# Optimization experiments

Measured on AMD Instinct MI355X. Metric: run time of the kernel, lower is better.

Reference implementation:

```python
import jax, jax.numpy as jnp
import numpy as np

HIDDEN = 1024
NUM_HEADS = 16
HEAD_DIM = HIDDEN // NUM_HEADS


def setup_inputs() -> dict:
    key = jax.random.key(0)
    ks = jax.random.split(key, 9)
    s = 0.02
    return {
        "x": jax.random.normal(ks[0], (2, 2048, HIDDEN), dtype=jnp.float32),
        "wq": jax.random.normal(ks[1], (HIDDEN, HIDDEN), dtype=jnp.float32) * s,
        "bq": jnp.zeros((HIDDEN,), dtype=jnp.float32),
        "wk": jax.random.normal(ks[2], (HIDDEN, HIDDEN), dtype=jnp.float32) * s,
        "bk": jnp.zeros((HIDDEN,), dtype=jnp.float32),
        "wv": jax.random.normal(ks[3], (HIDDEN, HIDDEN), dtype=jnp.float32) * s,
        "bv": jnp.zeros((HIDDEN,), dtype=jnp.float32),
        "wo": jax.random.normal(ks[4], (HIDDEN, HIDDEN), dtype=jnp.float32) * s,
        "bo": jnp.zeros((HIDDEN,), dtype=jnp.float32),
    }


def reference(x, wq, bq, wk, bk, wv, bv, wo, bo):
    B, S, H = x.shape
    # torch nn.Linear: y = x @ W.T + b
    q = x @ wq.T + bq
    k = x @ wk.T + bk
    v = x @ wv.T + bv
    # [B, S, nH, dH] -> [B, nH, S, dH]
    q = q.reshape(B, S, NUM_HEADS, HEAD_DIM).transpose(0, 2, 1, 3)
    k = k.reshape(B, S, NUM_HEADS, HEAD_DIM).transpose(0, 2, 1, 3)
    v = v.reshape(B, S, NUM_HEADS, HEAD_DIM).transpose(0, 2, 1, 3)
    scores = jnp.einsum("bhqd,bhkd->bhqk", q, k)
    probs = jax.nn.softmax(scores / jnp.sqrt(jnp.float32(HEAD_DIM)), axis=-1)
    context = jnp.einsum("bhqk,bhkd->bhqd", probs, v)
    context = context.transpose(0, 2, 1, 3).reshape(B, S, H)
    return context @ wo.T + bo
```

## Files before the change

### kernel.cpp

```cpp
#include <hip/hip_runtime.h>
#include <math.h>

#define HID   1024
#define NHEAD 16
#define DHEAD 64
#define BATCH 2
#define SEQ   2048
#define TOK   (BATCH*SEQ)

typedef float f32x4  __attribute__((ext_vector_type(4)));
typedef short short8 __attribute__((ext_vector_type(8)));

__device__ __forceinline__ unsigned short f2bf(float f) {
    unsigned int u = __float_as_uint(f);
    u += 0x7FFFu + ((u >> 16) & 1u);
    return (unsigned short)(u >> 16);
}

__global__ __launch_bounds__(256) void cvt_bf16(const float* __restrict__ in,
                                                unsigned short* __restrict__ out, int n8) {
    int i = blockIdx.x * 256 + threadIdx.x;
    if (i >= n8) return;
    const float4* p = (const float4*)in;
    float4 a = p[2*i], b = p[2*i+1];
    uint4 r;
    r.x = (unsigned)f2bf(a.x) | ((unsigned)f2bf(a.y) << 16);
    r.y = (unsigned)f2bf(a.z) | ((unsigned)f2bf(a.w) << 16);
    r.z = (unsigned)f2bf(b.x) | ((unsigned)f2bf(b.y) << 16);
    r.w = (unsigned)f2bf(b.z) | ((unsigned)f2bf(b.w) << 16);
    ((uint4*)out)[i] = r;
}

template<int NZ, bool OUTF32>
__global__ __launch_bounds__(256) void gemm128(
    const unsigned short* __restrict__ A,
    const unsigned short* __restrict__ W0, const unsigned short* __restrict__ W1,
    const unsigned short* __restrict__ W2,
    const float* __restrict__ b0, const float* __restrict__ b1, const float* __restrict__ b2,
    void* __restrict__ C0, void* __restrict__ C1, void* __restrict__ C2,
    int M, int N, int K)
{
    __shared__ unsigned short As[128][40];
    __shared__ unsigned short Ws[128][40];
    const unsigned short* W = W0; const float* bias = b0; void* C = C0;
    if (NZ > 1) {
        int z = blockIdx.z;
        W    = (z==0) ? W0 : ((z==1) ? W1 : W2);
        bias = (z==0) ? b0 : ((z==1) ? b1 : b2);
        C    = (z==0) ? C0 : ((z==1) ? C1 : C2);
    }
    const int tid  = threadIdx.x;
    const int l15  = tid & 15, quad = (tid >> 4) & 3, w = tid >> 6;
    const int wm   = (w >> 1) * 64, wn = (w & 1) * 64;
    const int m0   = blockIdx.y * 128, n0 = blockIdx.x * 128;
    const int sr   = tid >> 2, sc = (tid & 3) * 8;

    f32x4 acc[4][4] = {};

    for (int k0 = 0; k0 < K; k0 += 32) {
        uint4 a0 = *(const uint4*)(A + (size_t)(m0+sr   )*K + k0 + sc);
        uint4 a1 = *(const uint4*)(A + (size_t)(m0+sr+64)*K + k0 + sc);
        uint4 w0 = *(const uint4*)(W + (size_t)(n0+sr   )*K + k0 + sc);
        uint4 w1 = *(const uint4*)(W + (size_t)(n0+sr+64)*K + k0 + sc);
        __syncthreads();
        *(uint4*)&As[sr   ][sc] = a0;
        *(uint4*)&As[sr+64][sc] = a1;
        *(uint4*)&Ws[sr   ][sc] = w0;
        *(uint4*)&Ws[sr+64][sc] = w1;
        __syncthreads();
        short8 af[4], bfv[4];
        #pragma unroll
        for (int mi = 0; mi < 4; ++mi) af[mi]  = *(const short8*)&As[wm + mi*16 + l15][quad*8];
        #pragma unroll
        for (int ni = 0; ni < 4; ++ni) bfv[ni] = *(const short8*)&Ws[wn + ni*16 + l15][quad*8];
        #pragma unroll
        for (int mi = 0; mi < 4; ++mi)
            #pragma unroll
            for (int ni = 0; ni < 4; ++ni)
                acc[mi][ni] = __builtin_amdgcn_mfma_f32_16x16x32_bf16(af[mi], bfv[ni], acc[mi][ni], 0, 0, 0);
    }

    float bv[4];
    #pragma unroll
    for (int ni = 0; ni < 4; ++ni) bv[ni] = bias[n0 + wn + ni*16 + l15];
    #pragma unroll
    for (int mi = 0; mi < 4; ++mi)
        #pragma unroll
        for (int ni = 0; ni < 4; ++ni)
            #pragma unroll
            for (int r = 0; r < 4; ++r) {
                const int row = m0 + wm + mi*16 + quad*4 + r;
                const int col = n0 + wn + ni*16 + l15;
                const float val = acc[mi][ni][r] + bv[ni];
                if (OUTF32) ((float*)C)[(size_t)row*N + col] = val;
                else ((unsigned short*)C)[(size_t)row*N + col] = f2bf(val);
            }
}

__global__ __launch_bounds__(256) void attn_mfma(
    const unsigned short* __restrict__ Qg, const unsigned short* __restrict__ Kg,
    const unsigned short* __restrict__ Vg, unsigned short* __restrict__ Og)
{
    __shared__ unsigned short Qs[128][72];
    __shared__ unsigned short Ks[64][72];
    __shared__ unsigned short VT[64][72];
    __shared__ unsigned short Pw[4][32][72];

    const int tid  = threadIdx.x;
    const int l15  = tid & 15, quad = (tid >> 4) & 3, w = tid >> 6;
    const int b    = blockIdx.z, h = blockIdx.y;
    const int q0   = blockIdx.x * 128;
    const size_t rowbase = (size_t)b * SEQ;
    const int    cbase   = h * DHEAD;

    {
        const int r = tid >> 1, c = (tid & 1) * 32;
        const unsigned short* src = Qg + (rowbase + q0 + r) * HID + cbase + c;
        *(uint4*)&Qs[r][c     ] = *(const uint4*)(src);
        *(uint4*)&Qs[r][c +  8] = *(const uint4*)(src + 8);
        *(uint4*)&Qs[r][c + 16] = *(const uint4*)(src + 16);
        *(uint4*)&Qs[r][c + 24] = *(const uint4*)(src + 24);
    }
    __syncthreads();

    short8 qa[2][2];
    #pragma unroll
    for (int mi = 0; mi < 2; ++mi)
        #pragma unroll
        for (int slab = 0; slab < 2; ++slab)
            qa[mi][slab] = *(const short8*)&Qs[w*32 + mi*16 + l15][slab*32 + quad*8];

    f32x4 o[2][4] = {};
    float l_acc[2][4] = {};

    for (int kt = 0; kt < SEQ/64; ++kt) {
        __syncthreads();
        {
            const int r = tid >> 2, c = (tid & 3) * 16;
            const unsigned short* src = Kg + (rowbase + kt*64 + r) * HID + cbase + c;
            *(uint4*)&Ks[r][c    ] = *(const uint4*)src;
            *(uint4*)&Ks[r][c + 8] = *(const uint4*)(src + 8);
        }
        {
            const int d = tid & 63;
            #pragma unroll
            for (int p = 0; p < 2; ++p) {
                const int kk = ((tid >> 6) * 8) + p * 32;
                const unsigned short* src = Vg + (rowbase + kt*64 + kk) * HID + cbase + d;
                unsigned int pk[4];
                #pragma unroll
                for (int j = 0; j < 4; ++j) {
                    unsigned int lo = src[(size_t)(2*j    ) * HID];
                    unsigned int hi = src[(size_t)(2*j + 1) * HID];
                    pk[j] = lo | (hi << 16);
                }
                uint4 v4; v4.x = pk[0]; v4.y = pk[1]; v4.z = pk[2]; v4.w = pk[3];
                *(uint4*)&VT[d][kk] = v4;
            }
        }
        __syncthreads();

        f32x4 s[2][4] = {};
        #pragma unroll
        for (int slab = 0; slab < 2; ++slab) {
            short8 kf[4];
            #pragma unroll
            for (int nt = 0; nt < 4; ++nt)
                kf[nt] = *(const short8*)&Ks[nt*16 + l15][slab*32 + quad*8];
            #pragma unroll
            for (int mi = 0; mi < 2; ++mi)
                #pragma unroll
                for (int nt = 0; nt < 4; ++nt)
                    s[mi][nt] = __builtin_amdgcn_mfma_f32_16x16x32_bf16(qa[mi][slab], kf[nt], s[mi][nt], 0, 0, 0);
        }

        #pragma unroll
        for (int mi = 0; mi < 2; ++mi)
            #pragma unroll
            for (int nt = 0; nt < 4; ++nt) {
                const f32x4 sv = s[mi][nt];
                #pragma unroll
                for (int r = 0; r < 4; ++r) {
                    const float p = __expf(sv[r] * 0.125f);
                    l_acc[mi][r] += p;
                    Pw[w][mi*16 + quad*4 + r][nt*16 + l15] = f2bf(p);
                }
            }

        #pragma unroll
        for (int slab = 0; slab < 2; ++slab) {
            short8 pa[2], vf[4];
            #pragma unroll
            for (int mi = 0; mi < 2; ++mi)
                pa[mi] = *(const short8*)&Pw[w][mi*16 + l15][slab*32 + quad*8];
            #pragma unroll
            for (int nt = 0; nt < 4; ++nt)
                vf[nt] = *(const short8*)&VT[nt*16 + l15][slab*32 + quad*8];
            #pragma unroll
            for (int mi = 0; mi < 2; ++mi)
                #pragma unroll
                for (int nt = 0; nt < 4; ++nt)
                    o[mi][nt] = __builtin_amdgcn_mfma_f32_16x16x32_bf16(pa[mi], vf[nt], o[mi][nt], 0, 0, 0);
        }
    }

    float linv[2][4];
    #pragma unroll
    for (int mi = 0; mi < 2; ++mi)
        #pragma unroll
        for (int r = 0; r < 4; ++r) {
            float l = l_acc[mi][r];
            l += __shfl_xor(l, 1, 16);
            l += __shfl_xor(l, 2, 16);
            l += __shfl_xor(l, 4, 16);
            l += __shfl_xor(l, 8, 16);
            linv[mi][r] = 1.0f / l;
        }
    #pragma unroll
    for (int mi = 0; mi < 2; ++mi)
        #pragma unroll
        for (int nt = 0; nt < 4; ++nt)
            #pragma unroll
            for (int r = 0; r < 4; ++r) {
                const size_t row = rowbase + q0 + w*32 + mi*16 + quad*4 + r;
                Og[row * HID + cbase + nt*16 + l15] = f2bf(o[mi][nt][r] * linv[mi][r]);
            }
}

extern "C" void kernel_launch(void* const* d_in, const int* in_sizes, int n_in,
                              void* d_out, int out_size, void* d_ws, size_t ws_size,
                              hipStream_t stream)
{
    const float* x  = (const float*)d_in[0];
    const float* wq = (const float*)d_in[1];
    const float* bq = (const float*)d_in[2];
    const float* wk = (const float*)d_in[3];
    const float* bk = (const float*)d_in[4];
    const float* wv = (const float*)d_in[5];
    const float* bv = (const float*)d_in[6];
    const float* wo = (const float*)d_in[7];
    const float* bo = (const float*)d_in[8];
    float* out = (float*)d_out;

    unsigned short* xb  = (unsigned short*)d_ws;
    unsigned short* wqb = xb  + (size_t)TOK * HID;
    unsigned short* wkb = wqb + (size_t)HID * HID;
    unsigned short* wvb = wkb + (size_t)HID * HID;
    unsigned short* wob = wvb + (size_t)HID * HID;
    unsigned short* qb  = wob + (size_t)HID * HID;
    unsigned short* kb  = qb  + (size_t)TOK * HID;
    unsigned short* vb  = kb  + (size_t)TOK * HID;
    unsigned short* cb  = vb  + (size_t)TOK * HID;

    const dim3 blk(256);
    cvt_bf16<<<dim3(TOK*HID/8/256), blk, 0, stream>>>(x,  xb,  TOK*HID/8);
    cvt_bf16<<<dim3(HID*HID/8/256), blk, 0, stream>>>(wq, wqb, HID*HID/8);
    cvt_bf16<<<dim3(HID*HID/8/256), blk, 0, stream>>>(wk, wkb, HID*HID/8);
    cvt_bf16<<<dim3(HID*HID/8/256), blk, 0, stream>>>(wv, wvb, HID*HID/8);
    cvt_bf16<<<dim3(HID*HID/8/256), blk, 0, stream>>>(wo, wob, HID*HID/8);

    gemm128<3, false><<<dim3(HID/128, TOK/128, 3), blk, 0, stream>>>(
        xb, wqb, wkb, wvb, bq, bk, bv, qb, kb, vb, TOK, HID, HID);

    attn_mfma<<<dim3(SEQ/128, NHEAD, BATCH), blk, 0, stream>>>(qb, kb, vb, cb);

    gemm128<1, true><<<dim3(HID/128, TOK/128, 1), blk, 0, stream>>>(
        cb, wob, wob, wob, bo, bo, bo, out, out, out, TOK, HID, HID);
}
```

Baseline: 237.7 us.

## Rework GEMM with direct LDS loads and attention with pre-transposed V, double buffering

The GEMM now stages tiles with global_load_lds into XOR-swizzled shared memory instead of going through registers. The QKV GEMM writes V pre-transposed per head so attention can load it with vector reads. Attention processes 256 queries per block with double-buffered K/V prefetch, swizzled LDS layouts and packed P writes via lane shuffles. The four weight conversions are merged into one launch. The attention grid shrinks to 256 blocks at one block per CU, which risks under-filling the device, and the new swizzled index math could hide correctness problems.

```diff
diff --git a/kernel.cpp b/kernel.cpp
--- a/kernel.cpp
+++ b/kernel.cpp
@@ -1,4 +1,5 @@
 #include <hip/hip_runtime.h>
+#include <hip/hip_bf16.h>
 #include <math.h>
 
 #define HID   1024
@@ -15,6 +16,18 @@
     unsigned int u = __float_as_uint(f);
     u += 0x7FFFu + ((u >> 16) & 1u);
     return (unsigned short)(u >> 16);
+}
+
+__device__ __forceinline__ unsigned pk2(float lo, float hi) {
+    union { __hip_bfloat162 h; unsigned u; } cv;
+    cv.h = __float22bfloat162_rn(make_float2(lo, hi));
+    return cv.u;
+}
+
+__device__ __forceinline__ void gll16(const unsigned short* g, unsigned short* l) {
+    __builtin_amdgcn_global_load_lds(
+        (const __attribute__((address_space(1))) void*)g,
+        (__attribute__((address_space(3))) void*)l, 16, 0, 0);
 }
 
 __global__ __launch_bounds__(256) void cvt_bf16(const float* __restrict__ in,
@@ -24,15 +37,31 @@
     const float4* p = (const float4*)in;
     float4 a = p[2*i], b = p[2*i+1];
     uint4 r;
-    r.x = (unsigned)f2bf(a.x) | ((unsigned)f2bf(a.y) << 16);
-    r.y = (unsigned)f2bf(a.z) | ((unsigned)f2bf(a.w) << 16);
-    r.z = (unsigned)f2bf(b.x) | ((unsigned)f2bf(b.y) << 16);
-    r.w = (unsigned)f2bf(b.z) | ((unsigned)f2bf(b.w) << 16);
+    r.x = pk2(a.x, a.y); r.y = pk2(a.z, a.w);
+    r.z = pk2(b.x, b.y); r.w = pk2(b.z, b.w);
     ((uint4*)out)[i] = r;
 }
 
+__global__ __launch_bounds__(256) void cvt_bf16_w4(
+    const float* __restrict__ i0, const float* __restrict__ i1,
+    const float* __restrict__ i2, const float* __restrict__ i3,
+    unsigned short* __restrict__ o0, unsigned short* __restrict__ o1,
+    unsigned short* __restrict__ o2, unsigned short* __restrict__ o3, int n8) {
+    int i = blockIdx.x * 256 + threadIdx.x;
+    if (i >= n8) return;
+    int z = blockIdx.y;
+    const float* in = (z==0)?i0:((z==1)?i1:((z==2)?i2:i3));
+    unsigned short* out = (z==0)?o0:((z==1)?o1:((z==2)?o2:o3));
+    const float4* p = (const float4*)in;
+    float4 a = p[2*i], b = p[2*i+1];
+    uint4 r;
+    r.x = pk2(a.x, a.y); r.y = pk2(a.z, a.w);
+    r.z = pk2(b.x, b.y); r.w = pk2(b.z, b.w);
+    ((uint4*)out)[i] = r;
+}
+
 template<int NZ, bool OUTF32>
-__global__ __launch_bounds__(256) void gemm128(
+__global__ __launch_bounds__(256, 3) void gemm_gll(
     const unsigned short* __restrict__ A,
     const unsigned short* __restrict__ W0, const unsigned short* __restrict__ W1,
     const unsigned short* __restrict__ W2,
@@ -40,11 +69,13 @@
     void* __restrict__ C0, void* __restrict__ C1, void* __restrict__ C2,
     int M, int N, int K)
 {
-    __shared__ unsigned short As[128][40];
-    __shared__ unsigned short Ws[128][40];
+    __shared__ unsigned short As[128*32];
+    __shared__ unsigned short Ws[128*32];
+
     const unsigned short* W = W0; const float* bias = b0; void* C = C0;
+    int z = 0;
     if (NZ > 1) {
-        int z = blockIdx.z;
+        z = blockIdx.z;
         W    = (z==0) ? W0 : ((z==1) ? W1 : W2);
         bias = (z==0) ? b0 : ((z==1) ? b1 : b2);
         C    = (z==0) ? C0 : ((z==1) ? C1 : C2);
@@ -53,163 +84,209 @@
     const int l15  = tid & 15, quad = (tid >> 4) & 3, w = tid >> 6;
     const int wm   = (w >> 1) * 64, wn = (w & 1) * 64;
     const int m0   = blockIdx.y * 128, n0 = blockIdx.x * 128;
-    const int sr   = tid >> 2, sc = (tid & 3) * 8;
+
+    const int lane = tid & 63, w4 = tid >> 6;
+    const int grow = lane >> 2;
+    const int gchk = (lane & 3) ^ (grow & 3);
+    const unsigned short* pa0 = A + (size_t)(m0      + w4*16 + grow) * K + gchk*8;
+    const unsigned short* pa1 = A + (size_t)(m0 + 64 + w4*16 + grow) * K + gchk*8;
+    const unsigned short* pw0 = W + (size_t)(n0      + w4*16 + grow) * K + gchk*8;
+    const unsigned short* pw1 = W + (size_t)(n0 + 64 + w4*16 + grow) * K + gchk*8;
+    unsigned short* lA0 = &As[(w4*16)      * 32];
+    unsigned short* lA1 = &As[(64 + w4*16) * 32];
+    unsigned short* lW0 = &Ws[(w4*16)      * 32];
+    unsigned short* lW1 = &Ws[(64 + w4*16) * 32];
+
+    const int rchk = ((l15 & 3) );
 
     f32x4 acc[4][4] = {};
 
     for (int k0 = 0; k0 < K; k0 += 32) {
-        uint4 a0 = *(const uint4*)(A + (size_t)(m0+sr   )*K + k0 + sc);
-        uint4 a1 = *(const uint4*)(A + (size_t)(m0+sr+64)*K + k0 + sc);
-        uint4 w0 = *(const uint4*)(W + (size_t)(n0+sr   )*K + k0 + sc);
-        uint4 w1 = *(const uint4*)(W + (size_t)(n0+sr+64)*K + k0 + sc);
+        gll16(pa0, lA0); gll16(pa1, lA1);
+        gll16(pw0, lW0); gll16(pw1, lW1);
+        pa0 += 32; pa1 += 32; pw0 += 32; pw1 += 32;
         __syncthreads();
-        *(uint4*)&As[sr   ][sc] = a0;
-        *(uint4*)&As[sr+64][sc] = a1;
-        *(uint4*)&Ws[sr   ][sc] = w0;
-        *(uint4*)&Ws[sr+64][sc] = w1;
-        __syncthreads();
+
         short8 af[4], bfv[4];
-        #pragma unroll
-        for (int mi = 0; mi < 4; ++mi) af[mi]  = *(const short8*)&As[wm + mi*16 + l15][quad*8];
-        #pragma unroll
-        for (int ni = 0; ni < 4; ++ni) bfv[ni] = *(const short8*)&Ws[wn + ni*16 + l15][quad*8];
+        const int co = (quad ^ rchk) * 8;
+        #pragma unroll
+        for (int mi = 0; mi < 4; ++mi) af[mi]  = *(const short8*)&As[(wm + mi*16 + l15)*32 + co];
+        #pragma unroll
+        for (int ni = 0; ni < 4; ++ni) bfv[ni] = *(const short8*)&Ws[(wn + ni*16 + l15)*32 + co];
         #pragma unroll
         for (int mi = 0; mi < 4; ++mi)
             #pragma unroll
             for (int ni = 0; ni < 4; ++ni)
                 acc[mi][ni] = __builtin_amdgcn_mfma_f32_16x16x32_bf16(af[mi], bfv[ni], acc[mi][ni], 0, 0, 0);
+        __syncthreads();
     }
 
     float bv[4];
     #pragma unroll
     for (int ni = 0; ni < 4; ++ni) bv[ni] = bias[n0 + wn + ni*16 + l15];
-    #pragma unroll
-    for (int mi = 0; mi < 4; ++mi)
-        #pragma unroll
-        for (int ni = 0; ni < 4; ++ni)
-            #pragma unroll
-            for (int r = 0; r < 4; ++r) {
-                const int row = m0 + wm + mi*16 + quad*4 + r;
-                const int col = n0 + wn + ni*16 + l15;
-                const float val = acc[mi][ni][r] + bv[ni];
-                if (OUTF32) ((float*)C)[(size_t)row*N + col] = val;
-                else ((unsigned short*)C)[(size_t)row*N + col] = f2bf(val);
+
+    if (NZ == 3 && z == 2) {
+        #pragma unroll
+        for (int mi = 0; mi < 4; ++mi)
+            #pragma unroll
+            for (int ni = 0; ni < 4; ++ni) {
+                const int row0 = m0 + wm + mi*16 + quad*4;
+                const int col  = n0 + wn + ni*16 + l15;
+                const int hh = col >> 6, dd = col & 63;
+                const int bb = row0 >> 11, ss = row0 & 2047;
+                ushort4 r4;
+                r4.x = f2bf(acc[mi][ni][0] + bv[ni]);
+                r4.y = f2bf(acc[mi][ni][1] + bv[ni]);
+                r4.z = f2bf(acc[mi][ni][2] + bv[ni]);
+                r4.w = f2bf(acc[mi][ni][3] + bv[ni]);
+                *(ushort4*)((unsigned short*)C + ((size_t)(bb*NHEAD + hh)*DHEAD + dd)*SEQ + ss) = r4;
             }
-}
-
-__global__ __launch_bounds__(256) void attn_mfma(
+    } else {
+        #pragma unroll
+        for (int mi = 0; mi < 4; ++mi)
+            #pragma unroll
+            for (int ni = 0; ni < 4; ++ni)
+                #pragma unroll
+                for (int r = 0; r < 4; ++r) {
+                    const int row = m0 + wm + mi*16 + quad*4 + r;
+                    const int col = n0 + wn + ni*16 + l15;
+                    const float val = acc[mi][ni][r] + bv[ni];
+                    if (OUTF32) ((float*)C)[(size_t)row*N + col] = val;
+                    else ((unsigned short*)C)[(size_t)row*N + col] = f2bf(val);
+                }
+    }
+}
+
+__global__ __launch_bounds__(256, 1) void attn_v3(
     const unsigned short* __restrict__ Qg, const unsigned short* __restrict__ Kg,
-    const unsigned short* __restrict__ Vg, unsigned short* __restrict__ Og)
+    const unsigned short* __restrict__ vT, unsigned short* __restrict__ Og)
 {
-    __shared__ unsigned short Qs[128][72];
-    __shared__ unsigned short Ks[64][72];
-    __shared__ unsigned short VT[64][72];
-    __shared__ unsigned short Pw[4][32][72];
+    __shared__ unsigned short Ks[2][64][64];
+    __shared__ unsigned short VT[2][64][64];
+    __shared__ unsigned short Pw[4][64][64];
+    unsigned short* Qs = &Pw[0][0][0];
 
     const int tid  = threadIdx.x;
     const int l15  = tid & 15, quad = (tid >> 4) & 3, w = tid >> 6;
     const int b    = blockIdx.z, h = blockIdx.y;
-    const int q0   = blockIdx.x * 128;
+    const int q0   = blockIdx.x * 256;
     const size_t rowbase = (size_t)b * SEQ;
     const int    cbase   = h * DHEAD;
+    const size_t vbase   = (size_t)(b*NHEAD + h) * DHEAD * SEQ;
 
     {
-        const int r = tid >> 1, c = (tid & 1) * 32;
-        const unsigned short* src = Qg + (rowbase + q0 + r) * HID + cbase + c;
-        *(uint4*)&Qs[r][c     ] = *(const uint4*)(src);
-        *(uint4*)&Qs[r][c +  8] = *(const uint4*)(src + 8);
-        *(uint4*)&Qs[r][c + 16] = *(const uint4*)(src + 16);
-        *(uint4*)&Qs[r][c + 24] = *(const uint4*)(src + 24);
-    }
-    __syncthreads();
-
-    short8 qa[2][2];
+        const unsigned short* src = Qg + (rowbase + q0 + tid) * HID + cbase;
+        #pragma unroll
+        for (int j = 0; j < 8; ++j)
+            *(uint4*)&Qs[tid*64 + ((j ^ (tid & 7)) * 8)] = *(const uint4*)(src + j*8);
+    }
+    short8 qa[4][2];
     #pragma unroll
-    for (int mi = 0; mi < 2; ++mi)
-        #pragma unroll
-        for (int slab = 0; slab < 2; ++slab)
-            qa[mi][slab] = *(const short8*)&Qs[w*32 + mi*16 + l15][slab*32 + quad*8];
-
-    f32x4 o[2][4] = {};
-    float l_acc[2][4] = {};
+    for (int mi = 0; mi < 4; ++mi)
+        #pragma unroll
+        for (int s2 = 0; s2 < 2; ++s2)
+            qa[mi][s2] = *(const short8*)&Qs[(w*64 + mi*16 + l15)*64 + (((s2*4 + quad) ^ (l15 & 7)) * 8)];
+
+    const int sr = tid >> 2, sc = (tid & 3) * 16;
+    const int c0 = (sc >> 3) ^ (sr & 7);
+    const int c1 = ((sc >> 3) + 1) ^ (sr & 7);
+    {
+        const unsigned short* ks = Kg + (rowbase + sr) * HID + cbase + sc;
+        const unsigned short* vs = vT + vbase + (size_t)sr * SEQ + sc;
+        *(uint4*)&Ks[0][sr][c0*8] = *(const uint4*)ks;
+        *(uint4*)&Ks[0][sr][c1*8] = *(const uint4*)(ks + 8);
+        *(uint4*)&VT[0][sr][c0*8] = *(const uint4*)vs;
+        *(uint4*)&VT[0][sr][c1*8] = *(const uint4*)(vs + 8);
+    }
+
+    f32x4 o[4][4] = {};
+    f32x4 lsum[4] = {};
+    const int fco = ((quad) ^ (l15 & 7));
 
     for (int kt = 0; kt < SEQ/64; ++kt) {
+        const int buf = kt & 1;
         __syncthreads();
-        {
-            const int r = tid >> 2, c = (tid & 3) * 16;
-            const unsigned short* src = Kg + (rowbase + kt*64 + r) * HID + cbase + c;
-            *(uint4*)&Ks[r][c    ] = *(const uint4*)src;
-            *(uint4*)&Ks[r][c + 8] = *(const uint4*)(src + 8);
-        }
-        {
-            const int d = tid & 63;
-            #pragma unroll
-            for (int p = 0; p < 2; ++p) {
-                const int kk = ((tid >> 6) * 8) + p * 32;
-                const unsigned short* src = Vg + (rowbase + kt*64 + kk) * HID + cbase + d;
-                unsigned int pk[4];
-                #pragma unroll
-                for (int j = 0; j < 4; ++j) {
-                    unsigned int lo = src[(size_t)(2*j    ) * HID];
-                    unsigned int hi = src[(size_t)(2*j + 1) * HID];
-                    pk[j] = lo | (hi << 16);
-                }
-                uint4 v4; v4.x = pk[0]; v4.y = pk[1]; v4.z = pk[2]; v4.w = pk[3];
-                *(uint4*)&VT[d][kk] = v4;
-            }
-        }
-        __syncthreads();
-
-        f32x4 s[2][4] = {};
-        #pragma unroll
-        for (int slab = 0; slab < 2; ++slab) {
+
+        uint4 kr0, kr1, vr0, vr1;
+        const bool pre = (kt + 1 < SEQ/64);
+        if (pre) {
+            const unsigned short* ks = Kg + (rowbase + (kt+1)*64 + sr) * HID + cbase + sc;
+            const unsigned short* vs = vT + vbase + (size_t)sr * SEQ + (kt+1)*64 + sc;
+            kr0 = *(const uint4*)ks; kr1 = *(const uint4*)(ks + 8);
+            vr0 = *(const uint4*)vs; vr1 = *(const uint4*)(vs + 8);
+        }
+
+        f32x4 s[4][4] = {};
+        #pragma unroll
+        for (int s2 = 0; s2 < 2; ++s2) {
             short8 kf[4];
             #pragma unroll
             for (int nt = 0; nt < 4; ++nt)
-                kf[nt] = *(const short8*)&Ks[nt*16 + l15][slab*32 + quad*8];
-            #pragma unroll
-            for (int mi = 0; mi < 2; ++mi)
+                kf[nt] = *(const short8*)&Ks[buf][nt*16 + l15][((s2*4 + quad) ^ (l15 & 7)) * 8];
+            #pragma unroll
+            for (int mi = 0; mi < 4; ++mi)
                 #pragma unroll
                 for (int nt = 0; nt < 4; ++nt)
-                    s[mi][nt] = __builtin_amdgcn_mfma_f32_16x16x32_bf16(qa[mi][slab], kf[nt], s[mi][nt], 0, 0, 0);
-        }
-
-        #pragma unroll
-        for (int mi = 0; mi < 2; ++mi)
+                    s[mi][nt] = __builtin_amdgcn_mfma_f32_16x16x32_bf16(qa[mi][s2], kf[nt], s[mi][nt], 0, 0, 0);
+        }
+
+        const int odd = l15 & 1;
+        #pragma unroll
+        for (int mi = 0; mi < 4; ++mi) {
             #pragma unroll
             for (int nt = 0; nt < 4; ++nt) {
-                const f32x4 sv = s[mi][nt];
-                #pragma unroll
-                for (int r = 0; r < 4; ++r) {
-                    const float p = __expf(sv[r] * 0.125f);
-                    l_acc[mi][r] += p;
-                    Pw[w][mi*16 + quad*4 + r][nt*16 + l15] = f2bf(p);
-                }
+                const float p0 = __expf(s[mi][nt][0] * 0.125f);
+                const float p1 = __expf(s[mi][nt][1] * 0.125f);
+                const float p2 = __expf(s[mi][nt][2] * 0.125f);
+                const float p3 = __expf(s[mi][nt][3] * 0.125f);
+                lsum[mi][0] += p0; lsum[mi][1] += p1;
+                lsum[mi][2] += p2; lsum[mi][3] += p3;
+                const float x0 = __shfl_xor(p0, 1);
+                const float x1 = __shfl_xor(p1, 1);
+                const float x2 = __shfl_xor(p2, 1);
+                const float x3 = __shfl_xor(p3, 1);
+                const unsigned da = odd ? pk2(x2, p2) : pk2(p0, x0);
+                const unsigned db = odd ? pk2(x3, p3) : pk2(p1, x1);
+                const int rb = mi*16 + quad*4 + odd*2;
+                const int cp = nt*16 + (l15 & ~1);
+                const int ch = cp >> 3;
+                const int in = (cp & 7);
+                *(unsigned*)&Pw[w][rb  ][((ch ^ ( rb      & 7)) * 8) + in] = da;
+                *(unsigned*)&Pw[w][rb+1][((ch ^ ((rb + 1) & 7)) * 8) + in] = db;
             }
-
-        #pragma unroll
-        for (int slab = 0; slab < 2; ++slab) {
-            short8 pa[2], vf[4];
-            #pragma unroll
-            for (int mi = 0; mi < 2; ++mi)
-                pa[mi] = *(const short8*)&Pw[w][mi*16 + l15][slab*32 + quad*8];
+        }
+
+        #pragma unroll
+        for (int s2 = 0; s2 < 2; ++s2) {
+            short8 pa[4], vf[4];
+            #pragma unroll
+            for (int mi = 0; mi < 4; ++mi)
+                pa[mi] = *(const short8*)&Pw[w][mi*16 + l15][((s2*4 + quad) ^ (l15 & 7)) * 8];
             #pragma unroll
             for (int nt = 0; nt < 4; ++nt)
-                vf[nt] = *(const short8*)&VT[nt*16 + l15][slab*32 + quad*8];
-            #pragma unroll
-            for (int mi = 0; mi < 2; ++mi)
+                vf[nt] = *(const short8*)&VT[buf][nt*16 + l15][((s2*4 + quad) ^ (l15 & 7)) * 8];
+            #pragma unroll
+            for (int mi = 0; mi < 4; ++mi)
                 #pragma unroll
                 for (int nt = 0; nt < 4; ++nt)
                     o[mi][nt] = __builtin_amdgcn_mfma_f32_16x16x32_bf16(pa[mi], vf[nt], o[mi][nt], 0, 0, 0);
         }
-    }
-
-    float linv[2][4];
+
+        if (pre) {
+            const int nb = buf ^ 1;
+            *(uint4*)&Ks[nb][sr][c0*8] = kr0;
+            *(uint4*)&Ks[nb][sr][c1*8] = kr1;
+            *(uint4*)&VT[nb][sr][c0*8] = vr0;
+            *(uint4*)&VT[nb][sr][c1*8] = vr1;
+        }
+    }
+
+    float linv[4][4];
     #pragma unroll
-    for (int mi = 0; mi < 2; ++mi)
+    for (int mi = 0; mi < 4; ++mi)
         #pragma unroll
         for (int r = 0; r < 4; ++r) {
-            float l = l_acc[mi][r];
+            float l = lsum[mi][r];
             l += __shfl_xor(l, 1, 16);
             l += __shfl_xor(l, 2, 16);
             l += __shfl_xor(l, 4, 16);
@@ -217,12 +294,12 @@
             linv[mi][r] = 1.0f / l;
         }
     #pragma unroll
-    for (int mi = 0; mi < 2; ++mi)
+    for (int mi = 0; mi < 4; ++mi)
         #pragma unroll
         for (int nt = 0; nt < 4; ++nt)
             #pragma unroll
             for (int r = 0; r < 4; ++r) {
-                const size_t row = rowbase + q0 + w*32 + mi*16 + quad*4 + r;
+                const size_t row = rowbase + q0 + w*64 + mi*16 + quad*4 + r;
                 Og[row * HID + cbase + nt*16 + l15] = f2bf(o[mi][nt][r] * linv[mi][r]);
             }
 }
@@ -249,21 +326,19 @@
     unsigned short* wob = wvb + (size_t)HID * HID;
     unsigned short* qb  = wob + (size_t)HID * HID;
     unsigned short* kb  = qb  + (size_t)TOK * HID;
-    unsigned short* vb  = kb  + (size_t)TOK * HID;
-    unsigned short* cb  = vb  + (size_t)TOK * HID;
+    unsigned short* vtb = kb  + (size_t)TOK * HID;
+    unsigned short* cb  = vtb + (size_t)TOK * HID;
 
     const dim3 blk(256);
-    cvt_bf16<<<dim3(TOK*HID/8/256), blk, 0, stream>>>(x,  xb,  TOK*HID/8);
-    cvt_bf16<<<dim3(HID*HID/8/256), blk, 0, stream>>>(wq, wqb, HID*HID/8);
-    cvt_bf16<<<dim3(HID*HID/8/256), blk, 0, stream>>>(wk, wkb, HID*HID/8);
-    cvt_bf16<<<dim3(HID*HID/8/256), blk, 0, stream>>>(wv, wvb, HID*HID/8);
-    cvt_bf16<<<dim3(HID*HID/8/256), blk, 0, stream>>>(wo, wob, HID*HID/8);
-
-    gemm128<3, false><<<dim3(HID/128, TOK/128, 3), blk, 0, stream>>>(
-        xb, wqb, wkb, wvb, bq, bk, bv, qb, kb, vb, TOK, HID, HID);
-
-    attn_mfma<<<dim3(SEQ/128, NHEAD, BATCH), blk, 0, stream>>>(qb, kb, vb, cb);
-
-    gemm128<1, true><<<dim3(HID/128, TOK/128, 1), blk, 0, stream>>>(
+    cvt_bf16<<<dim3(TOK*HID/8/256), blk, 0, stream>>>(x, xb, TOK*HID/8);
+    cvt_bf16_w4<<<dim3(HID*HID/8/256, 4), blk, 0, stream>>>(
+        wq, wk, wv, wo, wqb, wkb, wvb, wob, HID*HID/8);
+
+    gemm_gll<3, false><<<dim3(HID/128, TOK/128, 3), blk, 0, stream>>>(
+        xb, wqb, wkb, wvb, bq, bk, bv, qb, kb, vtb, TOK, HID, HID);
+
+    attn_v3<<<dim3(SEQ/256, NHEAD, BATCH), blk, 0, stream>>>(qb, kb, vtb, cb);
+
+    gemm_gll<1, true><<<dim3(HID/128, TOK/128, 1), blk, 0, stream>>>(
         cb, wob, wob, wob, bo, bo, bo, out, out, out, TOK, HID, HID);
 }
```

New measurement: 233.7 us. About the same (-1.7%).
